# Performance work log

Hardware: AMD Instinct MI355X
Metric: run time of the kernel (lower is better)

The kernel has to match this reference:

```python
import jax, jax.numpy as jnp
import numpy as np

BATCH = 16384
N_FEATURES = 768
FT_OUT = 1024
ACTIVE_P = 32.0 / 768.0  # ~32 active features per board, like real positions


def setup_inputs() -> dict:
    key = jax.random.key(0)
    k1, k2, k3, k4, k5, k6 = jax.random.split(key, 6)
    # densified sparse one-hot boards: binary {0,1} with ~32/768 density
    board_stm = (jax.random.uniform(k1, (BATCH, N_FEATURES)) < ACTIVE_P).astype(jnp.float32)
    board_nstm = (jax.random.uniform(k2, (BATCH, N_FEATURES)) < ACTIVE_P).astype(jnp.float32)
    # Linear(768, FT_OUT): weight [out, in], bias [out]
    W_ft = jax.random.normal(k3, (FT_OUT, N_FEATURES), dtype=jnp.float32) * (1.0 / np.sqrt(N_FEATURES))
    b_ft = jax.random.normal(k4, (FT_OUT,), dtype=jnp.float32) * 0.01
    # Linear(2*FT_OUT, 1)
    W_out = jax.random.normal(k5, (1, 2 * FT_OUT), dtype=jnp.float32) * (1.0 / np.sqrt(2 * FT_OUT))
    b_out = jax.random.normal(k6, (1,), dtype=jnp.float32) * 0.01
    return {"board_stm": board_stm, "board_nstm": board_nstm,
            "W_ft": W_ft, "b_ft": b_ft, "W_out": W_out, "b_out": b_out}


def screlu(x):
    # SCReLU: clamp(x, 0, 1)^2
    return jnp.square(jnp.clip(x, 0.0, 1.0))


def reference(board_stm, board_nstm, W_ft, b_ft, W_out, b_out):
    # feature transformer applied to both perspectives (shared weights)
    stm = jnp.einsum('bf,of->bo', board_stm, W_ft) + b_ft   # [B, FT_OUT]
    nstm = jnp.einsum('bf,of->bo', board_nstm, W_ft) + b_ft  # [B, FT_OUT]
    hidden = screlu(jnp.concatenate([stm, nstm], axis=1))    # [B, 2*FT_OUT]
    out = jnp.einsum('bh,oh->bo', hidden, W_out) + b_out     # [B, 1]
    return jax.nn.sigmoid(out)
```

## Files before the change

### kernel.cpp

```cpp
#include <hip/hip_runtime.h>
#include <stdint.h>

#define BATCH 16384
#define NF 768
#define FT 1024
#define RB 32
#define GR (2 * RB)
#define THREADS 1024
#define NW 16
#define ALD 80
#define NKS 12

typedef int i32x4 __attribute__((ext_vector_type(4)));

__global__ __launch_bounds__(192) void prep_wq(const float* __restrict__ W_ft,
                                               char* __restrict__ Wq,
                                               float* __restrict__ invs) {
    const int o = blockIdx.x;
    const int t = threadIdx.x;
    __shared__ float smax[3];
    __shared__ float sscale;
    const float4 v = *(const float4*)(W_ft + (size_t)o * NF + t * 4);
    float m = fmaxf(fmaxf(fabsf(v.x), fabsf(v.y)), fmaxf(fabsf(v.z), fabsf(v.w)));
    #pragma unroll
    for (int s = 32; s > 0; s >>= 1) m = fmaxf(m, __shfl_down(m, s, 64));
    if ((t & 63) == 0) smax[t >> 6] = m;
    __syncthreads();
    if (t == 0) {
        const float am = fmaxf(fmaxf(smax[0], smax[1]), smax[2]);
        sscale = 127.0f / am;
        invs[o] = am / 127.0f;
    }
    __syncthreads();
    const float s = sscale;
    const float arr[4] = {v.x, v.y, v.z, v.w};
    uint32_t pk = 0;
    #pragma unroll
    for (int j = 0; j < 4; ++j) {
        const int q = (int)rintf(arr[j] * s);
        pk |= ((uint32_t)(unsigned char)(char)q) << (8 * j);
    }
    *(uint32_t*)(Wq + (size_t)o * NF + t * 4) = pk;
}

__device__ __forceinline__ uint32_t pack01(float4 v) {
    return (uint32_t)(v.x != 0.0f) | ((uint32_t)(v.y != 0.0f) << 8)
         | ((uint32_t)(v.z != 0.0f) << 16) | ((uint32_t)(v.w != 0.0f) << 24);
}

__global__ __launch_bounds__(THREADS, 4) void nnue_mfma(
    const float* __restrict__ bstm, const float* __restrict__ bnstm,
    const char* __restrict__ Wq, const float* __restrict__ invs,
    const float* __restrict__ b_ft, const float* __restrict__ W_out,
    const float* __restrict__ b_out, float* __restrict__ out)
{
    __shared__ __align__(16) char Abuf[2][GR * ALD];
    __shared__ float red[GR][NW];

    const int t = threadIdx.x;
    const int w = t >> 6;
    const int l = t & 63;
    const int b0 = blockIdx.x * RB;

    const int srow = t >> 4;
    const int sseg = t & 15;
    const float* sbase = ((srow < RB) ? (bstm + (size_t)(b0 + srow) * NF)
                                      : (bnstm + (size_t)(b0 + srow - RB) * NF))
                         + sseg * 4;
    const int swr = srow * ALD + sseg * 4;

    *(uint32_t*)(&Abuf[0][swr]) = pack01(*(const float4*)sbase);
    __syncthreads();

    const int cl = l & 15;
    const int q = l >> 4;
    const char* bptr = Wq + (size_t)(w * 64 + cl) * NF + q * 16;
    const int aoff = cl * ALD + q * 16;

    i32x4 acc[4][4] = {};
    #pragma unroll 2
    for (int ks = 0; ks < NKS; ++ks) {
        const int cur = ks & 1;
        float4 nv;
        if (ks < NKS - 1) nv = *(const float4*)(sbase + (ks + 1) * 64);
        i32x4 bfrag[4];
        #pragma unroll
        for (int c = 0; c < 4; ++c)
            bfrag[c] = *(const i32x4*)(bptr + (size_t)c * 16 * NF + ks * 64);
        i32x4 afrag[4];
        #pragma unroll
        for (int r = 0; r < 4; ++r)
            afrag[r] = *(const i32x4*)(&Abuf[cur][aoff + r * 16 * ALD]);
        #pragma unroll
        for (int r = 0; r < 4; ++r)
            #pragma unroll
            for (int c = 0; c < 4; ++c)
                acc[r][c] = __builtin_amdgcn_mfma_i32_16x16x64_i8(
                    afrag[r], bfrag[c], acc[r][c], 0, 0, 0);
        if (ks < NKS - 1) *(uint32_t*)(&Abuf[cur ^ 1][swr]) = pack01(nv);
        __syncthreads();
    }

    float ps[4][4] = {};
    #pragma unroll
    for (int c = 0; c < 4; ++c) {
        const int col = w * 64 + c * 16 + cl;
        const float iv = invs[col];
        const float bf = b_ft[col];
        const float wo0 = W_out[col];
        const float wo1 = W_out[FT + col];
        #pragma unroll
        for (int r = 0; r < 4; ++r) {
            const float wo = (r < 2) ? wo0 : wo1;
            #pragma unroll
            for (int j = 0; j < 4; ++j) {
                float h = fmaf((float)acc[r][c][j], iv, bf);
                h = fminf(fmaxf(h, 0.0f), 1.0f);
                ps[r][j] = fmaf(h * h, wo, ps[r][j]);
            }
        }
    }
    #pragma unroll
    for (int r = 0; r < 4; ++r)
        #pragma unroll
        for (int j = 0; j < 4; ++j) {
            float v = ps[r][j];
            v += __shfl_xor(v, 1, 64);
            v += __shfl_xor(v, 2, 64);
            v += __shfl_xor(v, 4, 64);
            v += __shfl_xor(v, 8, 64);
            if (cl == 0) red[16 * r + 4 * q + j][w] = v;
        }
    __syncthreads();

    if (t < RB) {
        float x = b_out[0];
        #pragma unroll
        for (int w2 = 0; w2 < NW; ++w2)
            x += red[t][w2] + red[RB + t][w2];
        out[b0 + t] = 1.0f / (1.0f + expf(-x));
    }
}

extern "C" void kernel_launch(void* const* d_in, const int* in_sizes, int n_in,
                              void* d_out, int out_size, void* d_ws, size_t ws_size,
                              hipStream_t stream) {
    const float* board_stm  = (const float*)d_in[0];
    const float* board_nstm = (const float*)d_in[1];
    const float* W_ft       = (const float*)d_in[2];
    const float* b_ft       = (const float*)d_in[3];
    const float* W_out      = (const float*)d_in[4];
    const float* b_out      = (const float*)d_in[5];
    float* out = (float*)d_out;

    char* Wq = (char*)d_ws;
    float* invs = (float*)((char*)d_ws + (size_t)FT * NF);

    prep_wq<<<FT, 192, 0, stream>>>(W_ft, Wq, invs);
    nnue_mfma<<<BATCH / RB, THREADS, 0, stream>>>(board_stm, board_nstm, Wq, invs,
                                                  b_ft, W_out, b_out, out);
}
```

Before: 75.00 us.

## Stage full packed board tile in LDS upfront, drop per-k-step barriers

Instead of double-buffering a 64-column slice of the packed int8 boards per k-step with a __syncthreads each iteration, all threads load the whole 64x768 board tile up front (12 float4 loads each), pack it into LDS once, and sync once. The main MFMA loop then only reads LDS at a k-offset, with no barriers. This removes 12 block-wide syncs and the serialised load/pack per step. In exchange it uses about 49KB of LDS per block, which may cut occupancy, and it loses the overlap of board loads with the MFMA work.

```diff
diff --git a/kernel.cpp b/kernel.cpp
--- a/kernel.cpp
+++ b/kernel.cpp
@@ -8,7 +8,7 @@
 #define GR (2 * RB)
 #define THREADS 1024
 #define NW 16
-#define ALD 80
+#define ALD 784
 #define NKS 12
 
 typedef int i32x4 __attribute__((ext_vector_type(4)));
@@ -54,7 +54,7 @@
     const float* __restrict__ b_ft, const float* __restrict__ W_out,
     const float* __restrict__ b_out, float* __restrict__ out)
 {
-    __shared__ __align__(16) char Abuf[2][GR * ALD];
+    __shared__ __align__(16) char Albs[GR * ALD];
     __shared__ float red[GR][NW];
 
     const int t = threadIdx.x;
@@ -62,14 +62,21 @@
     const int l = t & 63;
     const int b0 = blockIdx.x * RB;
 
-    const int srow = t >> 4;
-    const int sseg = t & 15;
-    const float* sbase = ((srow < RB) ? (bstm + (size_t)(b0 + srow) * NF)
-                                      : (bnstm + (size_t)(b0 + srow - RB) * NF))
-                         + sseg * 4;
-    const int swr = srow * ALD + sseg * 4;
-
-    *(uint32_t*)(&Abuf[0][swr]) = pack01(*(const float4*)sbase);
+    float4 sv[12];
+    int srow[12], sc4[12];
+    #pragma unroll
+    for (int it = 0; it < 12; ++it) {
+        const int g = it * THREADS + t;
+        const int row = g / 192;
+        const int c4 = g - row * 192;
+        const float* src = (row < RB) ? (bstm + (size_t)(b0 + row) * NF)
+                                      : (bnstm + (size_t)(b0 + row - RB) * NF);
+        sv[it] = *(const float4*)(src + c4 * 4);
+        srow[it] = row; sc4[it] = c4;
+    }
+    #pragma unroll
+    for (int it = 0; it < 12; ++it)
+        *(uint32_t*)(&Albs[srow[it] * ALD + sc4[it] * 4]) = pack01(sv[it]);
     __syncthreads();
 
     const int cl = l & 15;
@@ -80,9 +87,6 @@
     i32x4 acc[4][4] = {};
     #pragma unroll 2
     for (int ks = 0; ks < NKS; ++ks) {
-        const int cur = ks & 1;
-        float4 nv;
-        if (ks < NKS - 1) nv = *(const float4*)(sbase + (ks + 1) * 64);
         i32x4 bfrag[4];
         #pragma unroll
         for (int c = 0; c < 4; ++c)
@@ -90,15 +94,13 @@
         i32x4 afrag[4];
         #pragma unroll
         for (int r = 0; r < 4; ++r)
-            afrag[r] = *(const i32x4*)(&Abuf[cur][aoff + r * 16 * ALD]);
+            afrag[r] = *(const i32x4*)(&Albs[aoff + r * 16 * ALD + ks * 64]);
         #pragma unroll
         for (int r = 0; r < 4; ++r)
             #pragma unroll
             for (int c = 0; c < 4; ++c)
                 acc[r][c] = __builtin_amdgcn_mfma_i32_16x16x64_i8(
                     afrag[r], bfrag[c], acc[r][c], 0, 0, 0);
-        if (ks < NKS - 1) *(uint32_t*)(&Abuf[cur ^ 1][swr]) = pack01(nv);
-        __syncthreads();
     }
 
     float ps[4][4] = {};
```

Result: no change. 75.06 us (+0.1%).
